# Kernel tuning notes

Measured on AMD Instinct MI355X. Metric: run time of the kernel, lower is better.

The kernel has to match this reference:

```python
import jax, jax.numpy as jnp
import numpy as np

NUM_HEADS = 4
NUM_GROUPS = 8
EPS = 1e-5


def group_norm(x, w, b):
    # x: [N, C, H, W], normalize over (C//G, H, W) per group
    N, C, H, W = x.shape
    xg = x.reshape(N, NUM_GROUPS, C // NUM_GROUPS, H, W)
    mu = jnp.mean(xg, axis=(2, 3, 4), keepdims=True)
    var = jnp.var(xg, axis=(2, 3, 4), keepdims=True)
    xn = ((xg - mu) * jax.lax.rsqrt(var + EPS)).reshape(N, C, H, W)
    return xn * w[None, :, None, None] + b[None, :, None, None]


def conv1x1(x, w, b):
    # x: [N, C, H, W], w: [Cout, Cin], b: [Cout]
    return jnp.einsum('nchw,dc->ndhw', x, w) + b[None, :, None, None]


def setup_inputs() -> dict:
    key = jax.random.key(0)
    ks = jax.random.split(key, 12)
    N, C, H, W = 2, 256, 64, 64
    s = 1.0 / np.sqrt(C)
    inp = {
        'x': jax.random.normal(ks[0], (N, C, H, W), jnp.float32),
        'mask': jax.random.randint(ks[1], (N, 1, H, W), 0, 2, jnp.int32),
        'norm_w': jnp.ones((C,), jnp.float32),
        'norm_b': jnp.zeros((C,), jnp.float32),
        'q_w': jax.random.normal(ks[2], (C, C), jnp.float32) * s,
        'q_b': jnp.zeros((C,), jnp.float32),
        'k_w': jax.random.normal(ks[3], (C, C), jnp.float32) * s,
        'k_b': jnp.zeros((C,), jnp.float32),
        'v_w': jax.random.normal(ks[4], (C, C), jnp.float32) * s,
        'v_b': jnp.zeros((C,), jnp.float32),
        'p_w': jax.random.normal(ks[5], (C, C), jnp.float32) * s,
        'p_b': jnp.zeros((C,), jnp.float32),
    }
    return inp


def reference(x, mask, norm_w, norm_b, q_w, q_b, k_w, k_b, v_w, v_b, p_w, p_b):
    N, C, H, W = x.shape
    hd = C // NUM_HEADS  # head dim
    L = H * W
    xn = group_norm(x, norm_w, norm_b)
    q = conv1x1(xn, q_w, q_b).reshape(N, NUM_HEADS, hd, L)
    k = conv1x1(xn, k_w, k_b).reshape(N, NUM_HEADS, hd, L)
    v = conv1x1(xn, v_w, v_b).reshape(N, NUM_HEADS, hd, L)
    scores = jnp.einsum('nhcl,nhck->nhlk', q, k) * (hd ** -0.5)
    probs = jax.nn.softmax(scores, axis=-1)
    out = jnp.einsum('nhlk,nhck->nhcl', probs, v).reshape(N, C, H, W)
    out = conv1x1(out, p_w, p_b)
    return (x + out, mask)
```

## Files before the change

kernel.cpp:

```cpp
#include <hip/hip_runtime.h>
#include <hip/hip_bf16.h>

#define NBATCH 2
#define CCH    256
#define LLEN   4096
#define NGROUP 8
#define CPG    32
#define NHEAD  4
#define HD     64
#define GEPS   1e-5f
#define QSCALE 0.18033688011112042f


typedef short bf16x8 __attribute__((ext_vector_type(8)));
typedef float f32x4  __attribute__((ext_vector_type(4)));

__device__ __forceinline__ unsigned short f2b(float f) {
  unsigned u = __float_as_uint(f);
  u += 0x7FFFu + ((u >> 16) & 1u);
  return (unsigned short)(u >> 16);
}
__device__ __forceinline__ unsigned pack2bf(float a, float b) {
  __hip_bfloat162 h = __float22bfloat162_rn(make_float2(a, b));
  union { __hip_bfloat162 h; unsigned u; } c;
  c.h = h;
  return c.u;
}
__device__ __forceinline__ float exp2_(float x) {
#if __has_builtin(__builtin_amdgcn_exp2f)
  return __builtin_amdgcn_exp2f(x);
#else
  return exp2f(x);
#endif
}

__global__ __launch_bounds__(256) void setup_kernel(
    const float* __restrict__ qw, const float* __restrict__ kw,
    const float* __restrict__ vw, const float* __restrict__ pw,
    const float* __restrict__ qb, const float* __restrict__ kb,
    const float* __restrict__ vb, const float* __restrict__ pb,
    const float* __restrict__ x, const int* __restrict__ mask,
    unsigned short* __restrict__ w16, float* __restrict__ bias_ws,
    float* __restrict__ part, float* __restrict__ out2) {
  __shared__ float rs[4], rss[4];
  const int b = blockIdx.x;
  const int t = threadIdx.x;
  if (b < 256) {
    const int idx = b * 256 + t;
    const int m = idx >> 14;
    const int rem = idx & 16383;
    const int cout = rem >> 6;
    const int ch4 = (rem & 63) << 2;
    const float* src[4] = {qw, kw, vw, pw};
    const float sc = (m == 0) ? QSCALE : 1.0f;
    const float4 v = ((const float4*)src[m])[(size_t)cout * 64 + (ch4 >> 2)];
    unsigned short* dst = w16 +
        ((size_t)(m * 16 + (cout >> 4)) * 8 + (ch4 >> 5)) * 512 +
        ((cout & 15) + 16 * ((ch4 >> 3) & 3)) * 8 + (ch4 & 7);
    dst[0] = f2b(v.x * sc); dst[1] = f2b(v.y * sc);
    dst[2] = f2b(v.z * sc); dst[3] = f2b(v.w * sc);
    if (b == 0) {
      bias_ws[t]       = qb[t] * QSCALE;
      bias_ws[256 + t] = kb[t];
      bias_ws[512 + t] = vb[t];
      bias_ws[768 + t] = pb[t];
    }
  } else if (b < 512) {
    const int sb = b - 256;
    const int gidx = sb >> 4, sub = sb & 15;
    const float4* xp = (const float4*)(x + (size_t)gidx * (CPG * LLEN)) + (size_t)sub * 2048;
    float s = 0.f, ss = 0.f;
    for (int i = t; i < 2048; i += 256) {
      const float4 v = xp[i];
      s += v.x + v.y + v.z + v.w;
      ss = fmaf(v.x, v.x, ss);
      ss = fmaf(v.y, v.y, ss);
      ss = fmaf(v.z, v.z, ss);
      ss = fmaf(v.w, v.w, ss);
    }
#pragma unroll
    for (int off = 32; off; off >>= 1) {
      s  += __shfl_down(s, off);
      ss += __shfl_down(ss, off);
    }
    if ((t & 63) == 0) { rs[t >> 6] = s; rss[t >> 6] = ss; }
    __syncthreads();
    if (t == 0) {
      part[sb * 2 + 0] = rs[0] + rs[1] + rs[2] + rs[3];
      part[sb * 2 + 1] = rss[0] + rss[1] + rss[2] + rss[3];
    }
  } else {
    const int i = (b - 512) * 256 + t;
    out2[i] = (float)mask[i];
  }
}

__global__ __launch_bounds__(256) void gn_apply_kernel(const float* __restrict__ x,
                                                       const float* __restrict__ w,
                                                       const float* __restrict__ b,
                                                       const float* __restrict__ part,
                                                       unsigned short* __restrict__ xn16) {
  const int l0 = blockIdx.x * 64, c0 = blockIdx.y * 32, n = blockIdx.z;
  const int g16 = n * 8 + blockIdx.y;
  float s = 0.f, ss = 0.f;
#pragma unroll
  for (int i = 0; i < 16; i++) {
    s  += part[(g16 * 16 + i) * 2 + 0];
    ss += part[(g16 * 16 + i) * 2 + 1];
  }
  const float inv_cnt = 1.0f / (float)(CPG * LLEN);
  const float mu = s * inv_cnt;
  const float rsg = rsqrtf(ss * inv_cnt - mu * mu + GEPS);
  __shared__ float tile[32][68];
  const int t = threadIdx.x;
  const int cl = t >> 3, l8 = t & 7;
  const float aa = rsg * w[c0 + cl];
  const float dd = b[c0 + cl] - mu * aa;
  const float* xrow = x + ((size_t)n * CCH + c0 + cl) * LLEN + l0;
#pragma unroll
  for (int i = 0; i < 2; i++) {
    const int ll = (l8 + 8 * i) * 4;
    float4 v = *(const float4*)(xrow + ll);
    v.x = fmaf(v.x, aa, dd);
    v.y = fmaf(v.y, aa, dd);
    v.z = fmaf(v.z, aa, dd);
    v.w = fmaf(v.w, aa, dd);
    *(float4*)&tile[cl][ll] = v;
  }
  __syncthreads();
  const int l = t & 63, cg = t >> 6;
  const int labs = l0 + l;
  bf16x8 ov;
#pragma unroll
  for (int j = 0; j < 8; j++) ov[j] = (short)f2b(tile[cg * 8 + j][l]);
  const size_t pos = (((size_t)n * 256 + (labs >> 4)) * 8 + (c0 >> 5)) * 512 +
                     ((labs & 15) + 16 * cg) * 8;
  *(bf16x8*)(xn16 + pos) = ov;
}

__global__ __launch_bounds__(256, 4) void qkv_mfma_kernel(
    const unsigned short* __restrict__ xn16,
    const unsigned short* __restrict__ w16,
    const float* __restrict__ bias_ws,
    unsigned short* __restrict__ q16,
    unsigned short* __restrict__ k16,
    unsigned short* __restrict__ v16) {
  const int t = threadIdx.x;
  const int lane = t & 63, wv = t >> 6;
  const int col = lane & 15, quad = lane >> 4;
  const int m0 = blockIdx.x * 64;
  const int by = blockIdx.y;
  const int co0 = by * 64;
  const int wsel = blockIdx.z;
  const int n = m0 >> 12;
  const int m16b = (m0 & 4095) >> 4;

  const unsigned short* xnb = xn16 + (size_t)n * (256 * 8 * 512);
  const unsigned short* wb  = w16 + ((size_t)(wsel * 16 + by * 4 + wv) * 8) * 512 + lane * 8;

  f32x4 acc[4];
#pragma unroll
  for (int i = 0; i < 4; i++) acc[i] = {0.f, 0.f, 0.f, 0.f};

#pragma unroll
  for (int kc = 0; kc < 8; kc++) {
    const bf16x8 wf = *(const bf16x8*)(wb + (size_t)kc * 512);
#pragma unroll
    for (int mt = 0; mt < 4; mt++) {
      const bf16x8 xf = *(const bf16x8*)(xnb + ((size_t)(m16b + mt) * 8 + kc) * 512 + lane * 8);
      acc[mt] = (wsel < 2)
          ? __builtin_amdgcn_mfma_f32_16x16x32_bf16(xf, wf, acc[mt], 0, 0, 0)
          : __builtin_amdgcn_mfma_f32_16x16x32_bf16(wf, xf, acc[mt], 0, 0, 0);
    }
  }

  if (wsel < 2) {
    unsigned short* dst = (wsel == 0) ? q16 : k16;
    const float bias = bias_ws[wsel * CCH + co0 + wv * 16 + col];
    const int lquad = (wv * 2 + (col >> 3)) & 3;
    const int j = col & 7;
#pragma unroll
    for (int mt = 0; mt < 4; mt++) {
      const size_t base = ((size_t)(n * 256 + m16b + mt) * 8 + by * 2 + (wv >> 1)) * 512 + j;
#pragma unroll
      for (int r = 0; r < 4; r++)
        dst[base + ((quad * 4 + r) + 16 * lquad) * 8] = f2b(acc[mt][r] + bias);
    }
  } else {
    const int l0 = m0 & 4095;
    const int j = col & 7;
#pragma unroll
    for (int ct = 0; ct < 4; ct++) {
      const size_t base = ((size_t)(n * 128 + (l0 >> 5) + (ct >> 1)) * 16 + by * 4 + wv) * 512 +
                          16 * (((ct & 1) << 1) + (col >> 3)) * 8 + j;
#pragma unroll
      for (int r = 0; r < 4; r++) {
        const int cout = co0 + wv * 16 + quad * 4 + r;
        v16[base + (quad * 4 + r) * 8] = f2b(acc[ct][r] + bias_ws[2 * CCH + cout]);
      }
    }
  }
}

__global__ __launch_bounds__(256, 2) void attn_mfma_kernel(
    const unsigned short* __restrict__ q16,
    const unsigned short* __restrict__ k16,
    const unsigned short* __restrict__ v16,
    unsigned short* __restrict__ o16) {
  __shared__ __align__(16) unsigned char shraw[20480];
  f32x4 (*red)[4][64] = (f32x4 (*)[4][64])shraw;
  f32x4 (*lred)[64] = (f32x4 (*)[64])(shraw + 16384);
  const int t = threadIdx.x;
  const int lane = t & 63, wv = t >> 6;
  const int col = lane & 15, quad = lane >> 4;
  const int fid = blockIdx.y * gridDim.x + blockIdx.x;
  const int nh = fid & 7, qx = fid >> 3;
  const int n = nh >> 2, h = nh & 3;
  const int hc = h * HD;
  const int qt0 = qx * 4;

  const unsigned short* qb = q16 + (size_t)n * (256 * 8 * 512);
  const unsigned short* kb = k16 + (size_t)n * (256 * 8 * 512);
  const unsigned short* vb = v16 + (size_t)n * (128 * 16 * 512);

  bf16x8 bq[4][2];
#pragma unroll
  for (int qt = 0; qt < 4; qt++)
#pragma unroll
    for (int ks = 0; ks < 2; ks++)
      bq[qt][ks] = *(const bf16x8*)(qb + ((size_t)(qt0 + qt) * 8 + h * 2 + ks) * 512 + lane * 8);

  bf16x8 bones;
#pragma unroll
  for (int i = 0; i < 8; i++) bones[i] = (short)0x3F80;

  f32x4 o[4][4], lacc[4];
#pragma unroll
  for (int qt = 0; qt < 4; qt++) {
    lacc[qt] = {0.f, 0.f, 0.f, 0.f};
#pragma unroll
    for (int ct = 0; ct < 4; ct++) o[qt][ct] = {0.f, 0.f, 0.f, 0.f};
  }

  auto ldK = [&](int kc0, int kt, int ks) {
    return *(const bf16x8*)(kb + ((size_t)((kc0 >> 4) + kt) * 8 + h * 2 + ks) * 512 + lane * 8);
  };
  auto ldV = [&](int kc0, int ct) {
    return *(const bf16x8*)(vb + ((size_t)(kc0 >> 5) * 16 + h * 4 + ct) * 512 + lane * 8);
  };

  bf16x8 kA[2][2], kB[2][2], vA[4], vB[4];
  auto loadK = [&](bf16x8 (&kr)[2][2], int kc0) {
#pragma unroll
    for (int kt = 0; kt < 2; kt++)
#pragma unroll
      for (int ks = 0; ks < 2; ks++) kr[kt][ks] = ldK(kc0, kt, ks);
  };
  auto loadV = [&](bf16x8 (&vv)[4], int kc0) {
#pragma unroll
    for (int ct = 0; ct < 4; ct++) vv[ct] = ldV(kc0, ct);
  };

  auto chunk = [&](bf16x8 (&kr)[2][2], bf16x8 (&vv)[4]) {
    bf16x8 pa[4];
#pragma unroll
    for (int qt = 0; qt < 4; qt++) {
      unsigned a0, a1, b0, b1;
      {
        f32x4 s = {0.f, 0.f, 0.f, 0.f};
        s = __builtin_amdgcn_mfma_f32_16x16x32_bf16(kr[0][0], bq[qt][0], s, 0, 0, 0);
        s = __builtin_amdgcn_mfma_f32_16x16x32_bf16(kr[0][1], bq[qt][1], s, 0, 0, 0);
        a0 = pack2bf(exp2_(s[0]), exp2_(s[1]));
        a1 = pack2bf(exp2_(s[2]), exp2_(s[3]));
      }
      {
        f32x4 s = {0.f, 0.f, 0.f, 0.f};
        s = __builtin_amdgcn_mfma_f32_16x16x32_bf16(kr[1][0], bq[qt][0], s, 0, 0, 0);
        s = __builtin_amdgcn_mfma_f32_16x16x32_bf16(kr[1][1], bq[qt][1], s, 0, 0, 0);
        b0 = pack2bf(exp2_(s[0]), exp2_(s[1]));
        b1 = pack2bf(exp2_(s[2]), exp2_(s[3]));
      }
      auto r0 = __builtin_amdgcn_permlane32_swap(a0, b0, false, false);
      auto s0 = __builtin_amdgcn_permlane16_swap(r0[0], r0[1], false, false);
      auto r1 = __builtin_amdgcn_permlane32_swap(a1, b1, false, false);
      auto s1 = __builtin_amdgcn_permlane16_swap(r1[0], r1[1], false, false);
      union { unsigned u[4]; bf16x8 v; } pu;
      pu.u[0] = s0[0];
      pu.u[1] = s1[0];
      pu.u[2] = s0[1];
      pu.u[3] = s1[1];
      pa[qt] = pu.v;
    }
    __builtin_amdgcn_s_setprio(1);
#pragma unroll
    for (int qt = 0; qt < 4; qt++) {
      lacc[qt] = __builtin_amdgcn_mfma_f32_16x16x32_bf16(pa[qt], bones, lacc[qt], 0, 0, 0);
#pragma unroll
      for (int ct = 0; ct < 4; ct++)
        o[qt][ct] = __builtin_amdgcn_mfma_f32_16x16x32_bf16(pa[qt], vv[ct], o[qt][ct], 0, 0, 0);
    }
    __builtin_amdgcn_s_setprio(0);
  };

  const int kb0 = wv * 1024;
  loadK(kA, kb0);
  loadV(vA, kb0);
  for (int it = 0; it < 32; it += 2) {
    loadK(kB, kb0 + (it + 1) * 32);
    loadV(vB, kb0 + (it + 1) * 32);
    chunk(kA, vA);
    const int nx = (it + 2 < 32) ? (it + 2) : (it + 1);
    loadK(kA, kb0 + nx * 32);
    loadV(vA, kb0 + nx * 32);
    chunk(kB, vB);
  }

  const int cch = hc + wv * 16 + col;
  const int lquad16 = 16 * ((cch >> 3) & 3);
  const size_t ctile = cch >> 5;
#pragma unroll
  for (int qt = 0; qt < 4; qt++) {
    __syncthreads();
#pragma unroll
    for (int ct = 0; ct < 4; ct++) red[wv][ct][lane] = o[qt][ct];
    lred[wv][lane] = lacc[qt];
    __syncthreads();
    f32x4 os = red[0][wv][lane];
    os += red[1][wv][lane];
    os += red[2][wv][lane];
    os += red[3][wv][lane];
    f32x4 ls = lred[0][lane];
    ls += lred[1][lane];
    ls += lred[2][lane];
    ls += lred[3][lane];
    const size_t base = (((size_t)n * 256 + qt0 + qt) * 8 + ctile) * 512 + (cch & 7);
#pragma unroll
    for (int r = 0; r < 4; r++)
      o16[base + ((quad * 4 + r) + lquad16) * 8] = f2b(os[r] / ls[r]);
  }
}

__global__ __launch_bounds__(256, 4) void proj_mfma_kernel(
    const unsigned short* __restrict__ o16,
    const unsigned short* __restrict__ w16,
    const float* __restrict__ pbias,
    const float* __restrict__ x,
    float* __restrict__ out) {
  const int t = threadIdx.x;
  const int lane = t & 63, wv = t >> 6;
  const int col = lane & 15, quad = lane >> 4;
  const int m0 = blockIdx.x * 32;
  const int by = blockIdx.y;
  const int co0 = by * 64;
  const int n = m0 >> 12, l0 = m0 & 4095;

  const unsigned short* ob = o16 + (size_t)n * (256 * 8 * 512);
  const unsigned short* wb = w16 + ((size_t)(48 + by * 4 + wv) * 8) * 512 + lane * 8;

  f32x4 acc[2];
#pragma unroll
  for (int i = 0; i < 2; i++) acc[i] = {0.f, 0.f, 0.f, 0.f};

#pragma unroll
  for (int kc = 0; kc < 8; kc++) {
    const bf16x8 aw = *(const bf16x8*)(wb + (size_t)kc * 512);
#pragma unroll
    for (int lt = 0; lt < 2; lt++) {
      const bf16x8 bo = *(const bf16x8*)(ob + ((size_t)((l0 >> 4) + lt) * 8 + kc) * 512 + lane * 8);
      acc[lt] = __builtin_amdgcn_mfma_f32_16x16x32_bf16(aw, bo, acc[lt], 0, 0, 0);
    }
  }
#pragma unroll
  for (int lt = 0; lt < 2; lt++)
#pragma unroll
    for (int r = 0; r < 4; r++) {
      const int cout = co0 + wv * 16 + quad * 4 + r;
      const size_t idx = ((size_t)(n * CCH + cout)) * LLEN + l0 + lt * 16 + col;
      out[idx] = acc[lt][r] + pbias[cout] + x[idx];
    }
}

extern "C" void kernel_launch(void* const* d_in, const int* in_sizes, int n_in,
                              void* d_out, int out_size, void* d_ws, size_t ws_size,
                              hipStream_t stream) {
  (void)in_sizes; (void)n_in; (void)out_size; (void)ws_size;
  const float* x      = (const float*)d_in[0];
  const int*   mask   = (const int*)d_in[1];
  const float* norm_w = (const float*)d_in[2];
  const float* norm_b = (const float*)d_in[3];
  const float* q_w    = (const float*)d_in[4];
  const float* q_b    = (const float*)d_in[5];
  const float* k_w    = (const float*)d_in[6];
  const float* k_b    = (const float*)d_in[7];
  const float* v_w    = (const float*)d_in[8];
  const float* v_b    = (const float*)d_in[9];
  const float* p_w    = (const float*)d_in[10];
  const float* p_b    = (const float*)d_in[11];

  const size_t TSZ = (size_t)NBATCH * LLEN * CCH;
  unsigned short* xn16 = (unsigned short*)d_ws;
  unsigned short* q16  = xn16 + TSZ;
  unsigned short* k16  = q16 + TSZ;
  unsigned short* v16  = k16 + TSZ;
  unsigned short* o16  = v16 + TSZ;
  unsigned short* w16  = o16 + TSZ;
  float* bias_ws = (float*)(w16 + 4 * 65536);
  float* part    = bias_ws + 1024;

  float* out  = (float*)d_out;
  float* out2 = out + TSZ;

  setup_kernel<<<544, 256, 0, stream>>>(q_w, k_w, v_w, p_w, q_b, k_b, v_b, p_b,
                                        x, mask, w16, bias_ws, part, out2);
  gn_apply_kernel<<<dim3(LLEN / 64, CCH / 32, NBATCH), 256, 0, stream>>>(
      x, norm_w, norm_b, part, xn16);
  qkv_mfma_kernel<<<dim3((NBATCH * LLEN) / 64, CCH / 64, 3), 256, 0, stream>>>(
      xn16, w16, bias_ws, q16, k16, v16);
  attn_mfma_kernel<<<dim3(LLEN / 64, NBATCH * NHEAD), 256, 0, stream>>>(
      q16, k16, v16, o16);
  proj_mfma_kernel<<<dim3((NBATCH * LLEN) / 32, CCH / 64), 256, 0, stream>>>(
      o16, w16, bias_ws + 768, x, out);
}
```

Before: 148.5 us.

## Retile QKV GEMM to full output channels per block; peel attention loop

The QKV projection kernel now has each block cover 32 positions and all 256 output channels of one weight, with each wave doing a 2x4 MFMA tile. The x fragments are reused across four weight tiles instead of one, which cuts redundant activation loads and drops the grid's channel dimension. The attention kernel now advances K/V pointers incrementally, peels the last iteration to remove the conditional next-index, and seeds the first score MFMA with a shared zero vector. Each wave holds more accumulators and loaded fragments, which raises register use and may lower occupancy.

```diff
diff --git a/kernel.cpp b/kernel.cpp
--- a/kernel.cpp
+++ b/kernel.cpp
@@ -148,55 +148,75 @@
   const int t = threadIdx.x;
   const int lane = t & 63, wv = t >> 6;
   const int col = lane & 15, quad = lane >> 4;
-  const int m0 = blockIdx.x * 64;
-  const int by = blockIdx.y;
-  const int co0 = by * 64;
-  const int wsel = blockIdx.z;
+  const int m0 = blockIdx.x * 32;
+  const int wsel = blockIdx.y;
   const int n = m0 >> 12;
   const int m16b = (m0 & 4095) >> 4;
-
-  const unsigned short* xnb = xn16 + (size_t)n * (256 * 8 * 512);
-  const unsigned short* wb  = w16 + ((size_t)(wsel * 16 + by * 4 + wv) * 8) * 512 + lane * 8;
-
-  f32x4 acc[4];
-#pragma unroll
-  for (int i = 0; i < 4; i++) acc[i] = {0.f, 0.f, 0.f, 0.f};
-
-#pragma unroll
-  for (int kc = 0; kc < 8; kc++) {
-    const bf16x8 wf = *(const bf16x8*)(wb + (size_t)kc * 512);
-#pragma unroll
-    for (int mt = 0; mt < 4; mt++) {
-      const bf16x8 xf = *(const bf16x8*)(xnb + ((size_t)(m16b + mt) * 8 + kc) * 512 + lane * 8);
-      acc[mt] = (wsel < 2)
-          ? __builtin_amdgcn_mfma_f32_16x16x32_bf16(xf, wf, acc[mt], 0, 0, 0)
-          : __builtin_amdgcn_mfma_f32_16x16x32_bf16(wf, xf, acc[mt], 0, 0, 0);
-    }
-  }
-
+  const int l0 = m0 & 4095;
+
+  const unsigned short* xnb = xn16 + (((size_t)n * 256 + m16b) * 8) * 512 + lane * 8;
+  const unsigned short* wb  = w16 + ((size_t)(wsel * 16 + wv * 4) * 8) * 512 + lane * 8;
+
+  f32x4 acc[2][4];
+#pragma unroll
+  for (int mt = 0; mt < 2; mt++)
+#pragma unroll
+    for (int ct = 0; ct < 4; ct++) acc[mt][ct] = {0.f, 0.f, 0.f, 0.f};
+
+  const int j = col & 7;
   if (wsel < 2) {
+#pragma unroll
+    for (int kc = 0; kc < 8; kc++) {
+      bf16x8 xf[2], wf[4];
+      xf[0] = *(const bf16x8*)(xnb + (size_t)kc * 512);
+      xf[1] = *(const bf16x8*)(xnb + (size_t)(8 + kc) * 512);
+#pragma unroll
+      for (int ct = 0; ct < 4; ct++)
+        wf[ct] = *(const bf16x8*)(wb + (size_t)(ct * 8 + kc) * 512);
+#pragma unroll
+      for (int mt = 0; mt < 2; mt++)
+#pragma unroll
+        for (int ct = 0; ct < 4; ct++)
+          acc[mt][ct] = __builtin_amdgcn_mfma_f32_16x16x32_bf16(xf[mt], wf[ct], acc[mt][ct], 0, 0, 0);
+    }
     unsigned short* dst = (wsel == 0) ? q16 : k16;
-    const float bias = bias_ws[wsel * CCH + co0 + wv * 16 + col];
-    const int lquad = (wv * 2 + (col >> 3)) & 3;
-    const int j = col & 7;
-#pragma unroll
-    for (int mt = 0; mt < 4; mt++) {
-      const size_t base = ((size_t)(n * 256 + m16b + mt) * 8 + by * 2 + (wv >> 1)) * 512 + j;
-#pragma unroll
-      for (int r = 0; r < 4; r++)
-        dst[base + ((quad * 4 + r) + 16 * lquad) * 8] = f2b(acc[mt][r] + bias);
+#pragma unroll
+    for (int ct = 0; ct < 4; ct++) {
+      const float bias = bias_ws[wsel * CCH + wv * 64 + ct * 16 + col];
+      const int lq = (ct & 1) * 2 + (col >> 3);
+#pragma unroll
+      for (int mt = 0; mt < 2; mt++) {
+        const size_t base = (((size_t)n * 256 + m16b + mt) * 8 + wv * 2 + (ct >> 1)) * 512 + j;
+#pragma unroll
+        for (int r = 0; r < 4; r++)
+          dst[base + ((quad * 4 + r) + 16 * lq) * 8] = f2b(acc[mt][ct][r] + bias);
+      }
     }
   } else {
-    const int l0 = m0 & 4095;
-    const int j = col & 7;
+#pragma unroll
+    for (int kc = 0; kc < 8; kc++) {
+      bf16x8 xf[2], wf[4];
+      xf[0] = *(const bf16x8*)(xnb + (size_t)kc * 512);
+      xf[1] = *(const bf16x8*)(xnb + (size_t)(8 + kc) * 512);
+#pragma unroll
+      for (int ct = 0; ct < 4; ct++)
+        wf[ct] = *(const bf16x8*)(wb + (size_t)(ct * 8 + kc) * 512);
+#pragma unroll
+      for (int mt = 0; mt < 2; mt++)
+#pragma unroll
+        for (int ct = 0; ct < 4; ct++)
+          acc[mt][ct] = __builtin_amdgcn_mfma_f32_16x16x32_bf16(wf[ct], xf[mt], acc[mt][ct], 0, 0, 0);
+    }
 #pragma unroll
     for (int ct = 0; ct < 4; ct++) {
-      const size_t base = ((size_t)(n * 128 + (l0 >> 5) + (ct >> 1)) * 16 + by * 4 + wv) * 512 +
-                          16 * (((ct & 1) << 1) + (col >> 3)) * 8 + j;
-#pragma unroll
-      for (int r = 0; r < 4; r++) {
-        const int cout = co0 + wv * 16 + quad * 4 + r;
-        v16[base + (quad * 4 + r) * 8] = f2b(acc[ct][r] + bias_ws[2 * CCH + cout]);
+      const size_t base = (((size_t)n * 128 + (l0 >> 5)) * 16 + wv * 4 + ct) * 512 + j;
+#pragma unroll
+      for (int mt = 0; mt < 2; mt++) {
+        const int lq = mt * 2 + (col >> 3);
+#pragma unroll
+        for (int r = 0; r < 4; r++)
+          v16[base + ((quad * 4 + r) + 16 * lq) * 8] =
+              f2b(acc[mt][ct][r] + bias_ws[2 * CCH + wv * 64 + ct * 16 + quad * 4 + r]);
       }
     }
   }
@@ -233,6 +253,7 @@
   bf16x8 bones;
 #pragma unroll
   for (int i = 0; i < 8; i++) bones[i] = (short)0x3F80;
+  const f32x4 zf = {0.f, 0.f, 0.f, 0.f};
 
   f32x4 o[4][4], lacc[4];
 #pragma unroll
@@ -242,23 +263,20 @@
     for (int ct = 0; ct < 4; ct++) o[qt][ct] = {0.f, 0.f, 0.f, 0.f};
   }
 
-  auto ldK = [&](int kc0, int kt, int ks) {
-    return *(const bf16x8*)(kb + ((size_t)((kc0 >> 4) + kt) * 8 + h * 2 + ks) * 512 + lane * 8);
+  const unsigned short* kp = kb + ((size_t)(wv * 64) * 8 + h * 2) * 512 + lane * 8;
+  const unsigned short* vp = vb + ((size_t)(wv * 32) * 16 + h * 4) * 512 + lane * 8;
+
+  bf16x8 kA[2][2], kB[2][2], vA[4], vB[4];
+  auto loadK = [&](bf16x8 (&kr)[2][2], const unsigned short* p) {
+#pragma unroll
+    for (int kt = 0; kt < 2; kt++)
+#pragma unroll
+      for (int ks = 0; ks < 2; ks++)
+        kr[kt][ks] = *(const bf16x8*)(p + kt * 4096 + ks * 512);
   };
-  auto ldV = [&](int kc0, int ct) {
-    return *(const bf16x8*)(vb + ((size_t)(kc0 >> 5) * 16 + h * 4 + ct) * 512 + lane * 8);
-  };
-
-  bf16x8 kA[2][2], kB[2][2], vA[4], vB[4];
-  auto loadK = [&](bf16x8 (&kr)[2][2], int kc0) {
-#pragma unroll
-    for (int kt = 0; kt < 2; kt++)
-#pragma unroll
-      for (int ks = 0; ks < 2; ks++) kr[kt][ks] = ldK(kc0, kt, ks);
-  };
-  auto loadV = [&](bf16x8 (&vv)[4], int kc0) {
-#pragma unroll
-    for (int ct = 0; ct < 4; ct++) vv[ct] = ldV(kc0, ct);
+  auto loadV = [&](bf16x8 (&vv)[4], const unsigned short* p) {
+#pragma unroll
+    for (int ct = 0; ct < 4; ct++) vv[ct] = *(const bf16x8*)(p + ct * 512);
   };
 
   auto chunk = [&](bf16x8 (&kr)[2][2], bf16x8 (&vv)[4]) {
@@ -267,15 +285,13 @@
     for (int qt = 0; qt < 4; qt++) {
       unsigned a0, a1, b0, b1;
       {
-        f32x4 s = {0.f, 0.f, 0.f, 0.f};
-        s = __builtin_amdgcn_mfma_f32_16x16x32_bf16(kr[0][0], bq[qt][0], s, 0, 0, 0);
+        f32x4 s = __builtin_amdgcn_mfma_f32_16x16x32_bf16(kr[0][0], bq[qt][0], zf, 0, 0, 0);
         s = __builtin_amdgcn_mfma_f32_16x16x32_bf16(kr[0][1], bq[qt][1], s, 0, 0, 0);
         a0 = pack2bf(exp2_(s[0]), exp2_(s[1]));
         a1 = pack2bf(exp2_(s[2]), exp2_(s[3]));
       }
       {
-        f32x4 s = {0.f, 0.f, 0.f, 0.f};
-        s = __builtin_amdgcn_mfma_f32_16x16x32_bf16(kr[1][0], bq[qt][0], s, 0, 0, 0);
+        f32x4 s = __builtin_amdgcn_mfma_f32_16x16x32_bf16(kr[1][0], bq[qt][0], zf, 0, 0, 0);
         s = __builtin_amdgcn_mfma_f32_16x16x32_bf16(kr[1][1], bq[qt][1], s, 0, 0, 0);
         b0 = pack2bf(exp2_(s[0]), exp2_(s[1]));
         b1 = pack2bf(exp2_(s[2]), exp2_(s[3]));
@@ -302,18 +318,22 @@
     __builtin_amdgcn_s_setprio(0);
   };
 
-  const int kb0 = wv * 1024;
-  loadK(kA, kb0);
-  loadV(vA, kb0);
-  for (int it = 0; it < 32; it += 2) {
-    loadK(kB, kb0 + (it + 1) * 32);
-    loadV(vB, kb0 + (it + 1) * 32);
+  loadK(kA, kp);
+  loadV(vA, vp);
+  for (int it = 0; it < 30; it += 2) {
+    loadK(kB, kp + 8192);
+    loadV(vB, vp + 8192);
     chunk(kA, vA);
-    const int nx = (it + 2 < 32) ? (it + 2) : (it + 1);
-    loadK(kA, kb0 + nx * 32);
-    loadV(vA, kb0 + nx * 32);
+    kp += 16384;
+    vp += 16384;
+    loadK(kA, kp);
+    loadV(vA, vp);
     chunk(kB, vB);
   }
+  loadK(kB, kp + 8192);
+  loadV(vB, vp + 8192);
+  chunk(kA, vA);
+  chunk(kB, vB);
 
   const int cch = hc + wv * 16 + col;
   const int lquad16 = 16 * ((cch >> 3) & 3);
@@ -414,7 +434,7 @@
                                         x, mask, w16, bias_ws, part, out2);
   gn_apply_kernel<<<dim3(LLEN / 64, CCH / 32, NBATCH), 256, 0, stream>>>(
       x, norm_w, norm_b, part, xn16);
-  qkv_mfma_kernel<<<dim3((NBATCH * LLEN) / 64, CCH / 64, 3), 256, 0, stream>>>(
+  qkv_mfma_kernel<<<dim3((NBATCH * LLEN) / 32, 3), 256, 0, stream>>>(
       xn16, w16, bias_ws, q16, k16, v16);
   attn_mfma_kernel<<<dim3(LLEN / 64, NBATCH * NHEAD), 256, 0, stream>>>(
       q16, k16, v16, o16);
```

After: 147.0 us. About the same (-1.0%).
